# Kernel optimization log

Measured on AMD Instinct MI355X. Metric: run time of the kernel, lower is better.

The kernel has to match this reference:

```python
import jax, jax.numpy as jnp
import numpy as np

N, E, D, HID, OUT, R = 100000, 640000, 128, 128, 128, 8


def setup_inputs() -> dict:
    key = jax.random.key(0)
    ks = jax.random.split(key, 12)
    x = jax.random.normal(ks[0], (N, D), dtype=jnp.float32)
    src = jax.random.randint(ks[1], (E,), 0, N)
    dst = jax.random.randint(ks[2], (E,), 0, N)
    etype = jax.random.randint(ks[3], (E,), 0, R)
    s = 0.05
    W_rel = jax.random.normal(ks[4], (R, D, OUT), dtype=jnp.float32) * s
    loop_w = jax.random.normal(ks[5], (D, OUT), dtype=jnp.float32) * s
    rel_bias = jax.random.normal(ks[6], (OUT,), dtype=jnp.float32) * s
    W1 = jax.random.normal(ks[7], (D + HID, 2 * HID), dtype=jnp.float32) * s
    b1 = jax.random.normal(ks[8], (2 * HID,), dtype=jnp.float32) * s
    W2 = jax.random.normal(ks[9], (D + 2 * HID, OUT), dtype=jnp.float32) * s
    b2 = jax.random.normal(ks[10], (OUT,), dtype=jnp.float32) * s
    return {"x": x, "src": src, "dst": dst, "etype": etype,
            "W_rel": W_rel, "loop_w": loop_w, "rel_bias": rel_bias,
            "W1": W1, "b1": b1, "W2": W2, "b2": b2}


def reference(x, src, dst, etype, W_rel, loop_w, rel_bias, W1, b1, W2, b2):
    n = x.shape[0]
    # RelGraphConv (low_mem): transform all nodes once per relation, then
    # gather the (relation, src)-specific message per edge.  [R, N, OUT]
    h_rel = jnp.einsum('nd,rdo->rno', x, W_rel)
    m = h_rel[etype, src]                                   # [E, OUT]
    agg = jax.ops.segment_sum(m, dst, num_segments=n)       # sum at dst
    msg = agg + x @ loop_w + rel_bias                       # self-loop + bias
    # concat-MLP update (is_block=False -> dst_x = x), activation = tanh
    mid = jnp.tanh(jnp.concatenate([x, msg], axis=1) @ W1 + b1)
    return jnp.concatenate([x, mid], axis=1) @ W2 + b2
```

## Files before the change

### kernel.cpp

```cpp
#include <hip/hip_runtime.h>

#define NN 100000
#define NE 640000
#define RR 8
#define NBIN 800000

typedef unsigned short u16;
typedef u16 u16x4 __attribute__((ext_vector_type(4)));
typedef u16 u16x8 __attribute__((ext_vector_type(8)));
typedef __bf16 bf16x8 __attribute__((ext_vector_type(8)));
typedef float f32x4 __attribute__((ext_vector_type(4)));

#define OFF_XB      0u
#define OFF_WT      25600000u
#define OFF_W1T     25894912u
#define OFF_W2T     26025984u
#define OFF_BUCKET  26124288u
#define OFF_CSROFF  28684288u
#define OFF_CUR     31884292u
#define OFF_PSUM    35084292u

__device__ inline u16 f2bf(float f) {
  unsigned u = __float_as_uint(f);
  u += 0x7FFF + ((u >> 16) & 1);
  return (u16)(u >> 16);
}
__device__ inline float bf2f(u16 h) { return __uint_as_float(((unsigned)h) << 16); }

__device__ inline int edge_bin(int d, int r) { return d * 8 + r; }

__global__ void k_cvt_x(const float* __restrict__ x, u16* __restrict__ xb) {
  const int i = (blockIdx.x * 256 + threadIdx.x) * 4;
  const float4 v = *(const float4*)(x + i);
  u16x4 o;
  o.x = f2bf(v.x); o.y = f2bf(v.y); o.z = f2bf(v.z); o.w = f2bf(v.w);
  *(u16x4*)(xb + i) = o;
}

__global__ void k_cvt_wrel(const float* __restrict__ W, const float* __restrict__ Lw,
                           u16* __restrict__ Wt) {
  const int idx = blockIdx.x * 256 + threadIdx.x;
  const int r = idx >> 14, o = (idx >> 7) & 127, d = idx & 127;
  Wt[idx] = f2bf(r < 8 ? W[(r << 14) + (d << 7) + o] : Lw[(d << 7) + o]);
}

__global__ void k_cvt_w1(const float* __restrict__ W1, u16* __restrict__ W1t) {
  const int idx = blockIdx.x * 256 + threadIdx.x;
  const int o = idx >> 8, i = idx & 255;
  W1t[idx] = f2bf(W1[i * 256 + o]);
}

__global__ void k_cvt_w2(const float* __restrict__ W2, u16* __restrict__ W2t) {
  const int idx = blockIdx.x * 256 + threadIdx.x;
  const int o = idx / 384, i = idx % 384;
  W2t[idx] = f2bf(W2[i * 128 + o]);
}

__global__ void k_hist(const int* __restrict__ dst, const int* __restrict__ et,
                       int* __restrict__ cnt) {
  const int e = blockIdx.x * 256 + threadIdx.x;
  if (e < NE) atomicAdd(&cnt[edge_bin(dst[e], et[e])], 1);
}

__global__ void k_scanA(const int* __restrict__ cnt, int* __restrict__ psum) {
  __shared__ int sc[256];
  const int tid = threadIdx.x, base = blockIdx.x * 1024 + tid * 4;
  int s = 0;
#pragma unroll
  for (int t = 0; t < 4; ++t) { const int i = base + t; if (i < NBIN) s += cnt[i]; }
  sc[tid] = s; __syncthreads();
  for (int d = 128; d > 0; d >>= 1) {
    if (tid < d) sc[tid] += sc[tid + d];
    __syncthreads();
  }
  if (tid == 0) psum[blockIdx.x] = sc[0];
}

__global__ void k_scanB(int* __restrict__ psum) {
  __shared__ int sc[1024];
  const int tid = threadIdx.x;
  const int v = (tid < 782) ? psum[tid] : 0;
  sc[tid] = v; __syncthreads();
  for (int d = 1; d < 1024; d <<= 1) {
    const int t = (tid >= d) ? sc[tid - d] : 0;
    __syncthreads();
    sc[tid] += t;
    __syncthreads();
  }
  if (tid < 782) psum[tid] = sc[tid] - v;
}

__global__ void k_scanC(int* __restrict__ cnt , const int* __restrict__ psum,
                        int* __restrict__ off) {
  __shared__ int sc[256];
  const int tid = threadIdx.x, base = blockIdx.x * 1024 + tid * 4;
  int c[4], s = 0;
#pragma unroll
  for (int t = 0; t < 4; ++t) {
    const int i = base + t;
    c[t] = (i < NBIN) ? cnt[i] : 0;
    s += c[t];
  }
  sc[tid] = s; __syncthreads();
  for (int d = 1; d < 256; d <<= 1) {
    const int t = (tid >= d) ? sc[tid - d] : 0;
    __syncthreads();
    sc[tid] += t;
    __syncthreads();
  }
  int run = psum[blockIdx.x] + sc[tid] - s;
#pragma unroll
  for (int t = 0; t < 4; ++t) {
    const int i = base + t;
    if (i < NBIN) { off[i] = run; cnt[i] = run; run += c[t]; }
  }
  if (blockIdx.x == 0 && tid == 0) off[NBIN] = NE;
}

__global__ void k_scatter(const int* __restrict__ src, const int* __restrict__ dst,
                          const int* __restrict__ et, int* __restrict__ cur,
                          unsigned* __restrict__ bucket) {
  const int e = blockIdx.x * 256 + threadIdx.x;
  if (e < NE) {
    const int d = dst[e], r = et[e];
    const int pos = atomicAdd(&cur[edge_bin(d, r)], 1);
    bucket[pos] = (unsigned)src[e] | ((unsigned)r << 17);
  }
}

#define ATS 136
#define WCAP 448
#define PDEP 6
__global__ __launch_bounds__(256, 4) void k_fused(
    const u16* __restrict__ xb, const u16* __restrict__ Wt,
    const int* __restrict__ csroff, const unsigned* __restrict__ bucket,
    const float* __restrict__ rel_bias,
    const u16* __restrict__ W1t, const float* __restrict__ b1,
    const u16* __restrict__ W2t, const float* __restrict__ b2,
    float* __restrict__ out) {
  __shared__ u16 At[4 * 32 * ATS];
  __shared__ unsigned wlds[WCAP];
  const int tid = threadIdx.x;
  const int v0 = blockIdx.x * 32;
  const int wave = tid >> 6, lane = tid & 63;
  const int l16 = lane & 15, quad = lane >> 4;
  const int rt = wave & 1, cb = (wave >> 1) << 6;
  const int si = tid >> 3, sj = tid & 7;

  const int gbase = csroff[v0 * 8];
  const int ntot  = csroff[v0 * 8 + 256] - gbase;

  f32x4 acc[4] = {};

  {
    const u16* xp = xb + ((size_t)(v0 + rt * 16 + l16) << 7) + quad * 8;
    bf16x8 afr[4];
#pragma unroll
    for (int t = 0; t < 4; ++t) afr[t] = *(const bf16x8*)(xp + t * 32);
    const u16* wb = Wt + (8 << 14);
#pragma unroll
    for (int c = 0; c < 4; ++c) {
      const u16* wp = wb + (size_t)(cb + c * 16 + l16) * 128 + quad * 8;
#pragma unroll
      for (int t = 0; t < 4; ++t)
        acc[c] = __builtin_amdgcn_mfma_f32_16x16x32_bf16(afr[t], *(const bf16x8*)(wp + t * 32), acc[c], 0, 0, 0);
    }
  }

  {
    const int nst = ntot < WCAP ? ntot : WCAP;
    for (int i = tid; i < nst; i += 256) wlds[i] = bucket[gbase + i];
  }
  __syncthreads();

#pragma unroll
  for (int ph = 0; ph < 2; ++ph) {
    {
      const u16x8 z = {0, 0, 0, 0, 0, 0, 0, 0};
#pragma unroll
      for (int q = 0; q < 4; ++q) {
        u16* dp = &At[q * (32 * ATS) + si * ATS + sj * 16];
        *(u16x8*)dp = z;
        *(u16x8*)(dp + 8) = z;
      }
    }

    {
      const int pbeg = csroff[v0 * 8 + si * 8 + ph * 4] - gbase;
      const int pend = csroff[v0 * 8 + si * 8 + ph * 4 + 4] - gbase;
      const int n = pend - pbeg;
      float a[16] = {};
      int crel = -1;
      unsigned wv[PDEP];
      u16x8 h0[PDEP], h1[PDEP];
#pragma unroll
      for (int j = 0; j < PDEP; ++j) {
        if (j < n) {
          const int p = pbeg + j;
          const unsigned w = (p < WCAP) ? wlds[p] : bucket[gbase + p];
          wv[j] = w;
          const u16* xp = xb + ((size_t)(w & 0x1FFFFu) << 7) + sj * 16;
          h0[j] = *(const u16x8*)xp;
          h1[j] = *(const u16x8*)(xp + 8);
        }
      }
      for (int ib = 0; ib < n; ib += PDEP) {
#pragma unroll
        for (int j = 0; j < PDEP; ++j) {
          const int i = ib + j;
          if (i < n) {
            const int r = (int)((wv[j] >> 17) & 7u);
            if (r != crel) {
              if (crel >= 0) {
                u16x8 o0, o1;
#pragma unroll
                for (int t = 0; t < 8; ++t) { o0[t] = f2bf(a[t]); o1[t] = f2bf(a[8 + t]); }
                u16* dp = &At[(crel & 3) * (32 * ATS) + si * ATS + sj * 16];
                *(u16x8*)dp = o0;
                *(u16x8*)(dp + 8) = o1;
              }
#pragma unroll
              for (int t = 0; t < 16; ++t) a[t] = 0.f;
              crel = r;
            }
#pragma unroll
            for (int t = 0; t < 8; ++t) { a[t] += bf2f(h0[j][t]); a[8 + t] += bf2f(h1[j][t]); }
            const int p = i + PDEP;
            if (p < n) {
              const int pp = pbeg + p;
              const unsigned w = (pp < WCAP) ? wlds[pp] : bucket[gbase + pp];
              wv[j] = w;
              const u16* xp = xb + ((size_t)(w & 0x1FFFFu) << 7) + sj * 16;
              h0[j] = *(const u16x8*)xp;
              h1[j] = *(const u16x8*)(xp + 8);
            }
          }
        }
      }
      if (crel >= 0) {
        u16x8 o0, o1;
#pragma unroll
        for (int t = 0; t < 8; ++t) { o0[t] = f2bf(a[t]); o1[t] = f2bf(a[8 + t]); }
        u16* dp = &At[(crel & 3) * (32 * ATS) + si * ATS + sj * 16];
        *(u16x8*)dp = o0;
        *(u16x8*)(dp + 8) = o1;
      }
    }
    __syncthreads();

#pragma unroll
    for (int q = 0; q < 4; ++q) {
      bf16x8 afr[4];
#pragma unroll
      for (int t = 0; t < 4; ++t)
        afr[t] = *(const bf16x8*)&At[q * (32 * ATS) + (rt * 16 + l16) * ATS + quad * 8 + t * 32];
      const u16* wb = Wt + ((ph * 4 + q) << 14);
#pragma unroll
      for (int c = 0; c < 4; ++c) {
        const u16* wp = wb + (size_t)(cb + c * 16 + l16) * 128 + quad * 8;
#pragma unroll
        for (int t = 0; t < 4; ++t)
          acc[c] = __builtin_amdgcn_mfma_f32_16x16x32_bf16(afr[t], *(const bf16x8*)(wp + t * 32), acc[c], 0, 0, 0);
      }
    }
    __syncthreads();
  }

  u16* Mt = At;
  u16* Ht = At + 32 * 136;
#pragma unroll
  for (int c = 0; c < 4; ++c) {
    const int col = cb + c * 16 + l16;
    const float bias = rel_bias[col];
#pragma unroll
    for (int reg = 0; reg < 4; ++reg) {
      const int row = rt * 16 + quad * 4 + reg;
      Mt[row * 136 + col] = f2bf(acc[c][reg] + bias);
    }
  }
  __syncthreads();

  {
    const int ch = (wave >> 1) << 7;
    f32x4 acc2[8] = {};
#pragma unroll
    for (int kt = 0; kt < 8; ++kt) {
      bf16x8 af;
      if (kt < 4)
        af = *(const bf16x8*)(xb + ((size_t)(v0 + rt * 16 + l16) << 7) + kt * 32 + quad * 8);
      else
        af = *(const bf16x8*)&Mt[(rt * 16 + l16) * 136 + (kt - 4) * 32 + quad * 8];
#pragma unroll
      for (int ct = 0; ct < 8; ++ct) {
        const u16* wp = W1t + (size_t)(ch + ct * 16 + l16) * 256 + kt * 32 + quad * 8;
        acc2[ct] = __builtin_amdgcn_mfma_f32_16x16x32_bf16(af, *(const bf16x8*)(wp), acc2[ct], 0, 0, 0);
      }
    }
#pragma unroll
    for (int ct = 0; ct < 8; ++ct) {
      const int col = ch + ct * 16 + l16;
      const float bias = b1[col];
#pragma unroll
      for (int reg = 0; reg < 4; ++reg) {
        const int row = rt * 16 + quad * 4 + reg;
        Ht[row * 264 + col] = f2bf(tanhf(acc2[ct][reg] + bias));
      }
    }
  }
  __syncthreads();

  {
    f32x4 acc3[4] = {};
#pragma unroll
    for (int kt = 0; kt < 12; ++kt) {
      bf16x8 af;
      if (kt < 4)
        af = *(const bf16x8*)(xb + ((size_t)(v0 + rt * 16 + l16) << 7) + kt * 32 + quad * 8);
      else
        af = *(const bf16x8*)&Ht[(rt * 16 + l16) * 264 + (kt - 4) * 32 + quad * 8];
#pragma unroll
      for (int ct = 0; ct < 4; ++ct) {
        const u16* wp = W2t + (size_t)(cb + ct * 16 + l16) * 384 + kt * 32 + quad * 8;
        acc3[ct] = __builtin_amdgcn_mfma_f32_16x16x32_bf16(af, *(const bf16x8*)(wp), acc3[ct], 0, 0, 0);
      }
    }
#pragma unroll
    for (int ct = 0; ct < 4; ++ct) {
      const int col = cb + ct * 16 + l16;
      const float bias = b2[col];
#pragma unroll
      for (int reg = 0; reg < 4; ++reg) {
        const int row = v0 + rt * 16 + quad * 4 + reg;
        out[(size_t)row * 128 + col] = acc3[ct][reg] + bias;
      }
    }
  }
}

extern "C" void kernel_launch(void* const* d_in, const int* in_sizes, int n_in,
                              void* d_out, int out_size, void* d_ws, size_t ws_size,
                              hipStream_t stream) {
  (void)in_sizes; (void)n_in; (void)out_size; (void)ws_size;
  const float* x        = (const float*)d_in[0];
  const int*   src      = (const int*)d_in[1];
  const int*   dst      = (const int*)d_in[2];
  const int*   et       = (const int*)d_in[3];
  const float* W_rel    = (const float*)d_in[4];
  const float* loop_w   = (const float*)d_in[5];
  const float* rel_bias = (const float*)d_in[6];
  const float* W1       = (const float*)d_in[7];
  const float* b1       = (const float*)d_in[8];
  const float* W2       = (const float*)d_in[9];
  const float* b2       = (const float*)d_in[10];
  float* out = (float*)d_out;

  char* ws = (char*)d_ws;
  u16*      xb     = (u16*)(ws + OFF_XB);
  u16*      Wt     = (u16*)(ws + OFF_WT);
  u16*      W1t    = (u16*)(ws + OFF_W1T);
  u16*      W2t    = (u16*)(ws + OFF_W2T);
  unsigned* bucket = (unsigned*)(ws + OFF_BUCKET);
  int*      csroff = (int*)(ws + OFF_CSROFF);
  int*      cur    = (int*)(ws + OFF_CUR);
  int*      psum   = (int*)(ws + OFF_PSUM);

  hipMemsetAsync(cur, 0, (size_t)NBIN * 4, stream);

  k_cvt_x   <<<(NN * 128) / 1024, 256, 0, stream>>>(x, xb);
  k_cvt_wrel<<<(9 * 16384) / 256, 256, 0, stream>>>(W_rel, loop_w, Wt);
  k_cvt_w1  <<<(256 * 256) / 256, 256, 0, stream>>>(W1, W1t);
  k_cvt_w2  <<<(128 * 384) / 256, 256, 0, stream>>>(W2, W2t);

  k_hist    <<<(NE + 255) / 256, 256, 0, stream>>>(dst, et, cur);
  k_scanA   <<<782, 256, 0, stream>>>(cur, psum);
  k_scanB   <<<1, 1024, 0, stream>>>(psum);
  k_scanC   <<<782, 256, 0, stream>>>(cur, psum, csroff);
  k_scatter <<<(NE + 255) / 256, 256, 0, stream>>>(src, dst, et, cur, bucket);

  k_fused   <<<NN / 32, 256, 0, stream>>>(xb, Wt, csroff, bucket, rel_bias,
                                          W1t, b1, W2t, b2, out);
}
```

Before: 612.8 us.

## Aggregate one relation per phase with 16-lane node groups and smaller LDS

After: 611.2 us. Within noise of the previous version (-0.3%).

```diff
diff --git a/kernel.cpp b/kernel.cpp
--- a/kernel.cpp
+++ b/kernel.cpp
@@ -130,25 +130,35 @@
 
 #define ATS 136
 #define WCAP 448
-#define PDEP 6
-__global__ __launch_bounds__(256, 4) void k_fused(
+__global__ __launch_bounds__(256, 5) void k_fused(
     const u16* __restrict__ xb, const u16* __restrict__ Wt,
     const int* __restrict__ csroff, const unsigned* __restrict__ bucket,
     const float* __restrict__ rel_bias,
     const u16* __restrict__ W1t, const float* __restrict__ b1,
     const u16* __restrict__ W2t, const float* __restrict__ b2,
     float* __restrict__ out) {
-  __shared__ u16 At[4 * 32 * ATS];
+  __shared__ u16 smem[32 * 136 + 32 * 264];
   __shared__ unsigned wlds[WCAP];
+  __shared__ int coff[257];
   const int tid = threadIdx.x;
   const int v0 = blockIdx.x * 32;
   const int wave = tid >> 6, lane = tid & 63;
   const int l16 = lane & 15, quad = lane >> 4;
   const int rt = wave & 1, cb = (wave >> 1) << 6;
-  const int si = tid >> 3, sj = tid & 7;
+  const int grp = tid >> 4, l16g = tid & 15;
+
+  u16* At = smem;
+  u16* Mt = smem;
+  u16* Ht = smem + 32 * 136;
 
   const int gbase = csroff[v0 * 8];
   const int ntot  = csroff[v0 * 8 + 256] - gbase;
+
+  for (int i = tid; i < 257; i += 256) coff[i] = csroff[v0 * 8 + i];
+  {
+    const int nst = ntot < WCAP ? ntot : WCAP;
+    for (int i = tid; i < nst; i += 256) wlds[i] = bucket[gbase + i];
+  }
 
   f32x4 acc[4] = {};
 
@@ -166,95 +176,48 @@
         acc[c] = __builtin_amdgcn_mfma_f32_16x16x32_bf16(afr[t], *(const bf16x8*)(wp + t * 32), acc[c], 0, 0, 0);
     }
   }
-
-  {
-    const int nst = ntot < WCAP ? ntot : WCAP;
-    for (int i = tid; i < nst; i += 256) wlds[i] = bucket[gbase + i];
-  }
   __syncthreads();
 
-#pragma unroll
-  for (int ph = 0; ph < 2; ++ph) {
+  for (int ph = 0; ph < 8; ++ph) {
     {
-      const u16x8 z = {0, 0, 0, 0, 0, 0, 0, 0};
-#pragma unroll
-      for (int q = 0; q < 4; ++q) {
-        u16* dp = &At[q * (32 * ATS) + si * ATS + sj * 16];
-        *(u16x8*)dp = z;
-        *(u16x8*)(dp + 8) = z;
-      }
-    }
+      const int nodeA = grp, nodeB = grp + 16;
+      const int begA = coff[nodeA * 8 + ph] - gbase;
+      const int nA   = coff[nodeA * 8 + ph + 1] - gbase - begA;
+      const int begB = coff[nodeB * 8 + ph] - gbase;
+      const int nB   = coff[nodeB * 8 + ph + 1] - gbase - begB;
+      float a0[8] = {}, a1[8] = {};
+      const int nmax = nA > nB ? nA : nB;
+      for (int j = 0; j < nmax; ++j) {
+        const bool dA = j < nA, dB = j < nB;
+        unsigned wA = 0, wB = 0;
+        if (dA) { const int p = begA + j; wA = (p < WCAP) ? wlds[p] : bucket[gbase + p]; }
+        if (dB) { const int p = begB + j; wB = (p < WCAP) ? wlds[p] : bucket[gbase + p]; }
+        u16x8 hA, hB;
+        if (dA) hA = *(const u16x8*)(xb + ((size_t)(wA & 0x1FFFFu) << 7) + l16g * 8);
+        if (dB) hB = *(const u16x8*)(xb + ((size_t)(wB & 0x1FFFFu) << 7) + l16g * 8);
+        if (dA) {
+#pragma unroll
+          for (int u = 0; u < 8; ++u) a0[u] += bf2f(hA[u]);
+        }
+        if (dB) {
+#pragma unroll
+          for (int u = 0; u < 8; ++u) a1[u] += bf2f(hB[u]);
+        }
+      }
+      u16x8 o0, o1;
+#pragma unroll
+      for (int u = 0; u < 8; ++u) { o0[u] = f2bf(a0[u]); o1[u] = f2bf(a1[u]); }
+      *(u16x8*)&At[nodeA * ATS + l16g * 8] = o0;
+      *(u16x8*)&At[nodeB * ATS + l16g * 8] = o1;
+    }
+    __syncthreads();
 
     {
-      const int pbeg = csroff[v0 * 8 + si * 8 + ph * 4] - gbase;
-      const int pend = csroff[v0 * 8 + si * 8 + ph * 4 + 4] - gbase;
-      const int n = pend - pbeg;
-      float a[16] = {};
-      int crel = -1;
-      unsigned wv[PDEP];
-      u16x8 h0[PDEP], h1[PDEP];
-#pragma unroll
-      for (int j = 0; j < PDEP; ++j) {
-        if (j < n) {
-          const int p = pbeg + j;
-          const unsigned w = (p < WCAP) ? wlds[p] : bucket[gbase + p];
-          wv[j] = w;
-          const u16* xp = xb + ((size_t)(w & 0x1FFFFu) << 7) + sj * 16;
-          h0[j] = *(const u16x8*)xp;
-          h1[j] = *(const u16x8*)(xp + 8);
-        }
-      }
-      for (int ib = 0; ib < n; ib += PDEP) {
-#pragma unroll
-        for (int j = 0; j < PDEP; ++j) {
-          const int i = ib + j;
-          if (i < n) {
-            const int r = (int)((wv[j] >> 17) & 7u);
-            if (r != crel) {
-              if (crel >= 0) {
-                u16x8 o0, o1;
-#pragma unroll
-                for (int t = 0; t < 8; ++t) { o0[t] = f2bf(a[t]); o1[t] = f2bf(a[8 + t]); }
-                u16* dp = &At[(crel & 3) * (32 * ATS) + si * ATS + sj * 16];
-                *(u16x8*)dp = o0;
-                *(u16x8*)(dp + 8) = o1;
-              }
-#pragma unroll
-              for (int t = 0; t < 16; ++t) a[t] = 0.f;
-              crel = r;
-            }
-#pragma unroll
-            for (int t = 0; t < 8; ++t) { a[t] += bf2f(h0[j][t]); a[8 + t] += bf2f(h1[j][t]); }
-            const int p = i + PDEP;
-            if (p < n) {
-              const int pp = pbeg + p;
-              const unsigned w = (pp < WCAP) ? wlds[pp] : bucket[gbase + pp];
-              wv[j] = w;
-              const u16* xp = xb + ((size_t)(w & 0x1FFFFu) << 7) + sj * 16;
-              h0[j] = *(const u16x8*)xp;
-              h1[j] = *(const u16x8*)(xp + 8);
-            }
-          }
-        }
-      }
-      if (crel >= 0) {
-        u16x8 o0, o1;
-#pragma unroll
-        for (int t = 0; t < 8; ++t) { o0[t] = f2bf(a[t]); o1[t] = f2bf(a[8 + t]); }
-        u16* dp = &At[(crel & 3) * (32 * ATS) + si * ATS + sj * 16];
-        *(u16x8*)dp = o0;
-        *(u16x8*)(dp + 8) = o1;
-      }
-    }
-    __syncthreads();
-
-#pragma unroll
-    for (int q = 0; q < 4; ++q) {
       bf16x8 afr[4];
 #pragma unroll
       for (int t = 0; t < 4; ++t)
-        afr[t] = *(const bf16x8*)&At[q * (32 * ATS) + (rt * 16 + l16) * ATS + quad * 8 + t * 32];
-      const u16* wb = Wt + ((ph * 4 + q) << 14);
+        afr[t] = *(const bf16x8*)&At[(rt * 16 + l16) * ATS + quad * 8 + t * 32];
+      const u16* wb = Wt + (ph << 14);
 #pragma unroll
       for (int c = 0; c < 4; ++c) {
         const u16* wp = wb + (size_t)(cb + c * 16 + l16) * 128 + quad * 8;
@@ -266,8 +229,6 @@
     __syncthreads();
   }
 
-  u16* Mt = At;
-  u16* Ht = At + 32 * 136;
 #pragma unroll
   for (int c = 0; c < 4; ++c) {
     const int col = cb + c * 16 + l16;
@@ -296,6 +257,7 @@
         acc2[ct] = __builtin_amdgcn_mfma_f32_16x16x32_bf16(af, *(const bf16x8*)(wp), acc2[ct], 0, 0, 0);
       }
     }
+    __syncthreads();
 #pragma unroll
     for (int ct = 0; ct < 8; ++ct) {
       const int col = ch + ct * 16 + l16;
```
